# Kernel tuning notes

Hardware: AMD Instinct MI355X
Metric: run time of the kernel (lower is better)

The kernel has to match this reference:

```python
import jax, jax.numpy as jnp
import numpy as np

B, H, NC, CS, D = 4, 16, 64, 64, 64
BASE_LR = 1.0
EPS = 1e-6


def setup_inputs() -> dict:
    key = jax.random.key(0)
    ks = jax.random.split(key, 4)
    xk = jax.random.normal(ks[0], (B, H, NC, CS, D), jnp.float32)
    xv = jax.random.normal(ks[1], (B, H, NC, CS, D), jnp.float32)
    # weights/theta use the module's N(0, 0.02) init scale
    weight = 0.02 * jax.random.normal(ks[2], (H, D, D), jnp.float32)
    bias = jnp.zeros((H, 1, D), jnp.float32)
    gamma = jnp.ones((H, 1, D), jnp.float32)
    beta = jnp.zeros((H, 1, D), jnp.float32)
    theta = 0.02 * jax.random.normal(ks[3], (H, D, 1), jnp.float32)
    theta_bias = jnp.zeros((H, 1, 1), jnp.float32)
    alpha = jnp.zeros((CS,), jnp.float32)
    return dict(xk=xk, xv=xv, weight=weight, bias=bias, gamma=gamma,
                beta=beta, theta=theta, theta_bias=theta_bias, alpha=alpha)


def _ttt(xk, xv, weight, bias, gamma, beta, theta, theta_bias, alpha):
    Bq, Hq, NCq, CSq, Dq = xk.shape
    # TTTDynamicLearningGate: token_idx = clamp(1/arange + alpha, 0)
    token_idx = jnp.maximum(1.0 / jnp.arange(1, CSq + 1, dtype=xk.dtype) + alpha, 0.0)
    token_eta = token_idx[None, None, :, None]  # [1,1,CS,1]
    g = gamma[None]       # [1,H,1,D]
    bt = beta[None]       # [1,H,1,D]
    tb = theta_bias[None]  # [1,H,1,1]
    # detach(): tile slow weights over batch -> fast weights
    W0 = jnp.broadcast_to(weight[None], (Bq, Hq, Dq, Dq))
    b0 = jnp.broadcast_to(bias[None], (Bq, Hq, 1, Dq))

    def step(carry, chunk):
        W, b = carry
        xk_c, xv_c = chunk  # [B,H,CS,D]
        # lr gate: eta = token_eta * (base_lr * sigmoid(x @ theta + b) / head_dim)
        lr = jax.nn.sigmoid(jnp.einsum('bhkc,hcd->bhkd', xk_c, theta) + tb)
        eta = token_eta * (BASE_LR * lr / Dq)  # [B,H,CS,1]
        # forward through fast weights (depth = 1)
        z = xk_c @ W + b
        # multi-head LayerNorm, detailed
        mu = z.mean(-1, keepdims=True)
        var = ((z - mu) ** 2).mean(-1, keepdims=True)
        std = jnp.sqrt(var + EPS)
        x_hat = (z - mu) / std
        y = g * x_hat + bt
        # L2 reconstruction grad through LN (manual backward)
        grad_out = y - (xv_c - xk_c)
        gxh = grad_out * g
        grad_x = (Dq * gxh - gxh.sum(-1, keepdims=True)
                  - x_hat * (gxh * x_hat).sum(-1, keepdims=True)) / (Dq * std)
        # fast-weight delta + step()
        dW = jnp.einsum('bhkd,bhke->bhde', eta * xk_c, grad_x)
        db = (eta * grad_x).sum(-2, keepdims=True)
        Wn, bn = W - dW, b - db
        return (Wn, bn), xk_c @ Wn + bn

    chunks = (jnp.moveaxis(xk, 2, 0), jnp.moveaxis(xv, 2, 0))  # [NC,B,H,CS,D]
    (_, _), outs = jax.lax.scan(step, (W0, b0), chunks)
    return jnp.moveaxis(outs, 0, 2)  # [B,H,NC,CS,D]


def reference(xk, xv, weight, bias, gamma, beta, theta, theta_bias, alpha):
    return _ttt(xk, xv, weight, bias, gamma, beta, theta, theta_bias, alpha)
```

## Files before the change

### kernel.cpp

```cpp
#include <hip/hip_runtime.h>
#include <hip/hip_bf16.h>
#include <math.h>

#define NCC 64
#define CSC 64
#define DC 64
#define S 72
#define EPSF 1e-6f
#define LDS_BYTES 66816

typedef __attribute__((ext_vector_type(8))) short bf16x8;
typedef __attribute__((ext_vector_type(4))) float f32x4;
typedef __attribute__((ext_vector_type(4))) short short4v;
typedef __attribute__((ext_vector_type(2))) short short2v;

static __device__ __forceinline__ short cvt_bf16(float x) {
    union { __hip_bfloat16 b; short s; } u;
    u.b = __float2bfloat16(x);
    return u.s;
}
static __device__ __forceinline__ float bf16_to_f(unsigned hw) {
    union { unsigned u; float f; } v; v.u = hw << 16;
    return v.f;
}

#define DPP_ROR_ADD(v, N)                                                     \
    do {                                                                      \
        union { float f; int i; } _u, _r;                                     \
        _u.f = (v);                                                           \
        _r.i = __builtin_amdgcn_mov_dpp(_u.i, 0x120 + (N), 0xF, 0xF, true);   \
        (v) += _r.f;                                                          \
    } while (0)

static __device__ __forceinline__ float red16(float v) {
    DPP_ROR_ADD(v, 1);
    DPP_ROR_ADD(v, 2);
    DPP_ROR_ADD(v, 4);
    DPP_ROR_ADD(v, 8);
    return v;
}

__global__ __launch_bounds__(512, 1) void ttt_kernel(
    const float* __restrict__ xk, const float* __restrict__ xv,
    const float* __restrict__ weight, const float* __restrict__ bias,
    const float* __restrict__ gamma, const float* __restrict__ beta,
    const float* __restrict__ theta, const float* __restrict__ theta_bias,
    const float* __restrict__ alpha, float* __restrict__ out)
{
    extern __shared__ char sb[];
    auto xs_rm = (short (*)[CSC][S])(sb);
    auto xsT   = (short (*)[DC][S]) (sb + 18432);
    auto gsT   = (short (*)[S])     (sb + 36864);
    auto Gr    = (short (*)[S])     (sb + 46080);
    auto Wtb   = (short (*)[S])     (sb + 55296);
    auto dbp   = (float (*)[DC])    (sb + 64512);
    auto bs    = (float*)           (sb + 66560);

    const int t   = threadIdx.x;
    const int w   = t >> 6;
    const bool lo = (w < 4);
    const int ws  = w & 3;
    const int l   = t & 63;
    const int g   = l >> 4, la = l & 15;
    const int r0  = 16*ws + 4*g;
    const int io  = lo ? 0 : 2;
    const int ts  = 64*ws + l;
    const int bh  = blockIdx.x;
    const int h   = bh & 15;

    const size_t bh_off = (size_t)bh * NCC*CSC*DC;
    const float* xkb = xk + bh_off;
    const float* xvb = xv + bh_off;
    float*       ob  = out + bh_off;

    float gam[4], bet[4], thv[4];
#pragma unroll
    for (int n = 0; n < 4; ++n) {
        gam[n] = gamma[h*DC + 16*n + la];
        bet[n] = beta [h*DC + 16*n + la];
        thv[n] = theta[h*DC + 16*n + la];
    }
    const float tb = theta_bias[h];
    float tokk[2];
#pragma unroll
    for (int ii = 0; ii < 2; ++ii) {
        int r = r0 + io + ii;
        tokk[ii] = fmaxf(1.0f/(float)(r+1) + alpha[r], 0.0f);
    }
    if (t < DC) bs[t] = bias[h*DC + 16*(t & 3) + (t >> 2)];

    float Wreg[4][4];
    float4 xl[4];
    float xkh[4][4];
    float xvg[2][4];

#pragma unroll
    for (int ii = 0; ii < 2; ++ii)
#pragma unroll
        for (int n = 0; n < 4; ++n)
            xvg[ii][n] = xvb[(r0+io+ii)*DC + 16*n + la];

    if (lo) {
        const float* wg = weight + h*DC*DC;
#pragma unroll
        for (int i = 0; i < 4; ++i)
#pragma unroll
            for (int n = 0; n < 4; ++n)
                Wreg[i][n] = wg[(r0+i)*DC + 16*n + la];
#pragma unroll
        for (int n = 0; n < 4; ++n) {
            short4v sv;
#pragma unroll
            for (int i = 0; i < 4; ++i) sv[i] = cvt_bf16(Wreg[i][n]);
            *(short4v*)&Wtb[16*n + la][r0] = sv;
        }
#pragma unroll
        for (int i4 = 0; i4 < 4; ++i4) xl[i4] = ((const float4*)xkb)[ts + 256*i4];
#pragma unroll
        for (int i = 0; i < 4; ++i)
#pragma unroll
            for (int n = 0; n < 4; ++n)
                xkh[i][n] = xkb[(r0+i)*DC + 16*n + la];
#pragma unroll
        for (int i4 = 0; i4 < 4; ++i4) {
            int f = ts + 256*i4, k = f >> 4, j = f & 15;
            short4v s4;
            s4[0]=cvt_bf16(xl[i4].x); s4[1]=cvt_bf16(xl[i4].y);
            s4[2]=cvt_bf16(xl[i4].z); s4[3]=cvt_bf16(xl[i4].w);
            *(short4v*)&xs_rm[0][k][4*j] = s4;
        }
#pragma unroll
        for (int n = 0; n < 4; ++n) {
            short4v sv;
#pragma unroll
            for (int i = 0; i < 4; ++i) sv[i] = cvt_bf16(xkh[i][n]);
            *(short4v*)&xsT[0][16*n + la][r0] = sv;
        }
    }
    __syncthreads();

    for (int c = 0; c < NCC; ++c) {
        const int cb = c & 1, nb = cb ^ 1;
        const bool pf = (c + 1 < NCC);

        f32x4 bold = *(const f32x4*)&bs[4*la];

        const bf16x8 a0 = *(const bf16x8*)&xs_rm[cb][16*ws + la][8*g];
        const bf16x8 a1 = *(const bf16x8*)&xs_rm[cb][16*ws + la][32 + 8*g];
        f32x4 zt[4];
#pragma unroll
        for (int n = 0; n < 4; ++n) {
            bf16x8 w0 = *(const bf16x8*)&Wtb[16*n + la][8*g];
            bf16x8 w1 = *(const bf16x8*)&Wtb[16*n + la][32 + 8*g];
            f32x4 zz = {0.f,0.f,0.f,0.f};
            zz = __builtin_amdgcn_mfma_f32_16x16x32_bf16(a0, w0, zz, 0,0,0);
            zz = __builtin_amdgcn_mfma_f32_16x16x32_bf16(a1, w1, zz, 0,0,0);
            zt[n] = zz;
        }
        if (!lo) {
#pragma unroll
            for (int n = 0; n < 4; ++n) {
                bf16x8 b0 = *(const bf16x8*)&xs_rm[cb][16*n + la][8*g];
                bf16x8 b1 = *(const bf16x8*)&xs_rm[cb][16*n + la][32 + 8*g];
                f32x4 cc = {0.f,0.f,0.f,0.f};
                cc = __builtin_amdgcn_mfma_f32_16x16x32_bf16(a0, b0, cc, 0,0,0);
                cc = __builtin_amdgcn_mfma_f32_16x16x32_bf16(a1, b1, cc, 0,0,0);
                short4v sg;
#pragma unroll
                for (int i = 0; i < 4; ++i) sg[i] = cvt_bf16(-(cc[i] + 1.0f));
                *(short4v*)&Gr[16*n + la][r0] = sg;
            }
        }

        float xkq[2][4];
#pragma unroll
        for (int n = 0; n < 4; ++n) {
            unsigned pk = *(const unsigned*)&xsT[cb][16*n + la][r0 + io];
            xkq[0][n] = bf16_to_f(pk & 0xFFFFu);
            xkq[1][n] = bf16_to_f(pk >> 16);
        }

        float xvN[2][4];
        if (pf) {
            const float* xvn = xvb + (c+1)*CSC*DC;
#pragma unroll
            for (int ii = 0; ii < 2; ++ii)
#pragma unroll
                for (int n = 0; n < 4; ++n)
                    xvN[ii][n] = xvn[(r0+io+ii)*DC + 16*n + la];
            if (lo) {
                const float* xkn = xkb + (c+1)*CSC*DC;
#pragma unroll
                for (int i4 = 0; i4 < 4; ++i4) xl[i4] = ((const float4*)xkn)[ts + 256*i4];
#pragma unroll
                for (int i = 0; i < 4; ++i)
#pragma unroll
                    for (int n = 0; n < 4; ++n)
                        xkh[i][n] = xkn[(r0+i)*DC + 16*n + la];
            }
        }

        float zrow[2][4];
        if (lo) {
#pragma unroll
            for (int n = 0; n < 4; ++n) { zrow[0][n] = zt[n][0]; zrow[1][n] = zt[n][1]; }
        } else {
#pragma unroll
            for (int n = 0; n < 4; ++n) { zrow[0][n] = zt[n][2]; zrow[1][n] = zt[n][3]; }
        }

        float gsv[2][4];
#pragma unroll
        for (int ii = 0; ii < 2; ++ii) {
            float z4[4];
#pragma unroll
            for (int n = 0; n < 4; ++n) z4[n] = zrow[ii][n] + bold[n];
            float szz = red16(z4[0]*z4[0] + z4[1]*z4[1] + z4[2]*z4[2] + z4[3]*z4[3]);
            float sz  = red16(z4[0] + z4[1] + z4[2] + z4[3]);
            float thd = red16(xkq[ii][0]*thv[0] + xkq[ii][1]*thv[1] +
                              xkq[ii][2]*thv[2] + xkq[ii][3]*thv[3]);
            float mu   = sz * (1.0f/DC);
            float var  = szz*(1.0f/DC) - mu*mu;
            float rstd = rsqrtf(var + EPSF);
            float ex   = __expf(-(thd + tb));
            float lr   = __builtin_amdgcn_rcpf(1.0f + ex);
            float eta  = tokk[ii]*lr*(1.0f/DC);
            float xh[4], gxh[4], a1v = 0.f, a2v = 0.f;
#pragma unroll
            for (int n = 0; n < 4; ++n) {
                xh[n] = (z4[n]-mu)*rstd;
                float y  = fmaf(gam[n], xh[n], bet[n]);
                float go = y - xvg[ii][n] + xkq[ii][n];
                gxh[n] = go*gam[n];
                a1v += gxh[n];
                a2v = fmaf(gxh[n], xh[n], a2v);
            }
            float s1 = red16(a1v), s2 = red16(a2v);
            float sc = rstd*(1.0f/DC)*eta;
#pragma unroll
            for (int n = 0; n < 4; ++n)
                gsv[ii][n] = (64.f*gxh[n] - s1 - xh[n]*s2)*sc;
        }
#pragma unroll
        for (int n = 0; n < 4; ++n) {
            short2v sg;
            sg[0] = cvt_bf16(gsv[0][n]);
            sg[1] = cvt_bf16(gsv[1][n]);
            *(short2v*)&gsT[16*n + la][r0 + io] = sg;
        }
        float dbl[4];
#pragma unroll
        for (int n = 0; n < 4; ++n) {
            float dd = gsv[0][n] + gsv[1][n];
            dd += __shfl_xor(dd, 16);
            dd += __shfl_xor(dd, 32);
            dbl[n] = dd;
        }
        if (l < 16) {
            f32x4 dv = {dbl[0], dbl[1], dbl[2], dbl[3]};
            *(f32x4*)&dbp[w][4*la] = dv;
        }
        __syncthreads();

        if (lo) {
            const bf16x8 ax0 = *(const bf16x8*)&xsT[cb][16*ws + la][8*g];
            const bf16x8 ax1 = *(const bf16x8*)&xsT[cb][16*ws + la][32 + 8*g];
#pragma unroll
            for (int n = 0; n < 4; ++n) {
                bf16x8 q0 = *(const bf16x8*)&gsT[16*n + la][8*g];
                bf16x8 q1 = *(const bf16x8*)&gsT[16*n + la][32 + 8*g];
                f32x4 dw = {0.f,0.f,0.f,0.f};
                dw = __builtin_amdgcn_mfma_f32_16x16x32_bf16(ax0, q0, dw, 0,0,0);
                dw = __builtin_amdgcn_mfma_f32_16x16x32_bf16(ax1, q1, dw, 0,0,0);
                short4v sw;
#pragma unroll
                for (int i = 0; i < 4; ++i) {
                    Wreg[i][n] -= dw[i];
                    sw[i] = cvt_bf16(Wreg[i][n]);
                }
                *(short4v*)&Wtb[16*n + la][r0] = sw;
            }
            if (pf) {
#pragma unroll
                for (int i4 = 0; i4 < 4; ++i4) {
                    int f = ts + 256*i4, k = f >> 4, j = f & 15;
                    short4v s4;
                    s4[0]=cvt_bf16(xl[i4].x); s4[1]=cvt_bf16(xl[i4].y);
                    s4[2]=cvt_bf16(xl[i4].z); s4[3]=cvt_bf16(xl[i4].w);
                    *(short4v*)&xs_rm[nb][k][4*j] = s4;
                }
#pragma unroll
                for (int n = 0; n < 4; ++n) {
                    short4v sv;
#pragma unroll
                    for (int i = 0; i < 4; ++i) sv[i] = cvt_bf16(xkh[i][n]);
                    *(short4v*)&xsT[nb][16*n + la][r0] = sv;
                }
            }
            if (w == 0) {
                float s = dbp[0][l];
#pragma unroll
                for (int p = 1; p < 8; ++p) s += dbp[p][l];
                bs[l] -= s;
            }
        } else {
            const bf16x8 ar0 = *(const bf16x8*)&Gr[16*ws + la][8*g];
            const bf16x8 ar1 = *(const bf16x8*)&Gr[16*ws + la][32 + 8*g];
            float* oc = ob + c*CSC*DC;
#pragma unroll
            for (int n = 0; n < 4; ++n) {
                bf16x8 q0 = *(const bf16x8*)&gsT[16*n + la][8*g];
                bf16x8 q1 = *(const bf16x8*)&gsT[16*n + la][32 + 8*g];
                f32x4 og = zt[n];
                og = __builtin_amdgcn_mfma_f32_16x16x32_bf16(ar0, q0, og, 0,0,0);
                og = __builtin_amdgcn_mfma_f32_16x16x32_bf16(ar1, q1, og, 0,0,0);
#pragma unroll
                for (int i = 0; i < 4; ++i)
                    oc[(r0+i)*DC + 16*n + la] = og[i] + bold[n];
            }
        }
        if (pf) {
#pragma unroll
            for (int ii = 0; ii < 2; ++ii)
#pragma unroll
                for (int n = 0; n < 4; ++n)
                    xvg[ii][n] = xvN[ii][n];
        }
        __syncthreads();
    }
}

extern "C" void kernel_launch(void* const* d_in, const int* in_sizes, int n_in,
                              void* d_out, int out_size, void* d_ws, size_t ws_size,
                              hipStream_t stream) {
    const float* xk         = (const float*)d_in[0];
    const float* xv         = (const float*)d_in[1];
    const float* weight     = (const float*)d_in[2];
    const float* bias       = (const float*)d_in[3];
    const float* gamma      = (const float*)d_in[4];
    const float* beta       = (const float*)d_in[5];
    const float* theta      = (const float*)d_in[6];
    const float* theta_bias = (const float*)d_in[7];
    const float* alpha      = (const float*)d_in[8];
    float* out = (float*)d_out;

    (void)hipFuncSetAttribute((const void*)ttt_kernel,
                              hipFuncAttributeMaxDynamicSharedMemorySize,
                              LDS_BYTES);
    ttt_kernel<<<64, 512, LDS_BYTES, stream>>>(xk, xv, weight, bias, gamma, beta,
                                               theta, theta_bias, alpha, out);
}
```

Baseline: 141.2 us.

## Batch LayerNorm-backward reductions algebraically and move bias-grad reduction to output warps

Rewrites the LayerNorm backward so all row reductions (sum, sum of squares, theta dot, and gamma-weighted moments) are computed in one batch from z, then derives s1 and s2 in closed form. This removes the serial dependency of the second reduction round on mu/rstd, shortening the critical path of the per-chunk gradient step. It also drops the cross-lane shuffle reduction for the bias gradient, storing per-group partials to a larger LDS buffer, and has warp 4 (output side) do the final sum instead of warp 0. The trade-offs are more reductions overall, slightly different floating-point rounding, and more LDS use.

```diff
diff --git a/kernel.cpp b/kernel.cpp
--- a/kernel.cpp
+++ b/kernel.cpp
@@ -7,7 +7,7 @@
 #define DC 64
 #define S 72
 #define EPSF 1e-6f
-#define LDS_BYTES 66816
+#define LDS_BYTES 72960
 
 typedef __attribute__((ext_vector_type(8))) short bf16x8;
 typedef __attribute__((ext_vector_type(4))) float f32x4;
@@ -53,8 +53,8 @@
     auto gsT   = (short (*)[S])     (sb + 36864);
     auto Gr    = (short (*)[S])     (sb + 46080);
     auto Wtb   = (short (*)[S])     (sb + 55296);
-    auto dbp   = (float (*)[DC])    (sb + 64512);
-    auto bs    = (float*)           (sb + 66560);
+    auto dbp   = (float (*)[4][DC]) (sb + 64512);
+    auto bs    = (float*)           (sb + 72704);
 
     const int t   = threadIdx.x;
     const int w   = t >> 6;
@@ -87,6 +87,11 @@
         int r = r0 + io + ii;
         tokk[ii] = fmaxf(1.0f/(float)(r+1) + alpha[r], 0.0f);
     }
+    float a3p = 0.f;
+#pragma unroll
+    for (int n = 0; n < 4; ++n) a3p = fmaf(gam[n], gam[n], a3p);
+    const float A3 = red16(a3p);
+
     if (t < DC) bs[t] = bias[h*DC + 16*(t & 3) + (t >> 2)];
 
     float Wreg[4][4];
@@ -212,34 +217,46 @@
         float gsv[2][4];
 #pragma unroll
         for (int ii = 0; ii < 2; ++ii) {
-            float z4[4];
-#pragma unroll
-            for (int n = 0; n < 4; ++n) z4[n] = zrow[ii][n] + bold[n];
-            float szz = red16(z4[0]*z4[0] + z4[1]*z4[1] + z4[2]*z4[2] + z4[3]*z4[3]);
-            float sz  = red16(z4[0] + z4[1] + z4[2] + z4[3]);
-            float thd = red16(xkq[ii][0]*thv[0] + xkq[ii][1]*thv[1] +
-                              xkq[ii][2]*thv[2] + xkq[ii][3]*thv[3]);
+            float z4[4], cc4[4];
+#pragma unroll
+            for (int n = 0; n < 4; ++n) {
+                z4[n]  = zrow[ii][n] + bold[n];
+                cc4[n] = gam[n] * (bet[n] - xvg[ii][n] + xkq[ii][n]);
+            }
+            float p_sz=0.f, p_szz=0.f, p_thd=0.f, p_a1=0.f, p_a2=0.f, p_a4=0.f, p_a5=0.f;
+#pragma unroll
+            for (int n = 0; n < 4; ++n) {
+                float g2 = gam[n]*gam[n];
+                p_sz  += z4[n];
+                p_szz  = fmaf(z4[n], z4[n], p_szz);
+                p_thd  = fmaf(xkq[ii][n], thv[n], p_thd);
+                p_a1   = fmaf(g2, z4[n], p_a1);
+                p_a2   = fmaf(g2*z4[n], z4[n], p_a2);
+                p_a4  += cc4[n];
+                p_a5   = fmaf(cc4[n], z4[n], p_a5);
+            }
+            float sz  = red16(p_sz);
+            float szz = red16(p_szz);
+            float thd = red16(p_thd);
+            float A1  = red16(p_a1);
+            float A2  = red16(p_a2);
+            float A4  = red16(p_a4);
+            float A5  = red16(p_a5);
             float mu   = sz * (1.0f/DC);
             float var  = szz*(1.0f/DC) - mu*mu;
-            float rstd = rsqrtf(var + EPSF);
+            float r    = rsqrtf(var + EPSF);
             float ex   = __expf(-(thd + tb));
             float lr   = __builtin_amdgcn_rcpf(1.0f + ex);
             float eta  = tokk[ii]*lr*(1.0f/DC);
-            float xh[4], gxh[4], a1v = 0.f, a2v = 0.f;
-#pragma unroll
-            for (int n = 0; n < 4; ++n) {
-                xh[n] = (z4[n]-mu)*rstd;
-                float y  = fmaf(gam[n], xh[n], bet[n]);
-                float go = y - xvg[ii][n] + xkq[ii][n];
-                gxh[n] = go*gam[n];
-                a1v += gxh[n];
-                a2v = fmaf(gxh[n], xh[n], a2v);
-            }
-            float s1 = red16(a1v), s2 = red16(a2v);
-            float sc = rstd*(1.0f/DC)*eta;
-#pragma unroll
-            for (int n = 0; n < 4; ++n)
-                gsv[ii][n] = (64.f*gxh[n] - s1 - xh[n]*s2)*sc;
+            float s1 = fmaf(r, A1 - mu*A3, A4);
+            float s2 = r*r*(A2 - 2.0f*mu*A1 + mu*mu*A3) + r*(A5 - mu*A4);
+            float sc = r*(1.0f/DC)*eta;
+#pragma unroll
+            for (int n = 0; n < 4; ++n) {
+                float xh  = (z4[n]-mu)*r;
+                float gxh = fmaf(gam[n]*gam[n], xh, cc4[n]);
+                gsv[ii][n] = (64.f*gxh - s1 - xh*s2)*sc;
+            }
         }
 #pragma unroll
         for (int n = 0; n < 4; ++n) {
@@ -248,17 +265,11 @@
             sg[1] = cvt_bf16(gsv[1][n]);
             *(short2v*)&gsT[16*n + la][r0 + io] = sg;
         }
-        float dbl[4];
-#pragma unroll
-        for (int n = 0; n < 4; ++n) {
-            float dd = gsv[0][n] + gsv[1][n];
-            dd += __shfl_xor(dd, 16);
-            dd += __shfl_xor(dd, 32);
-            dbl[n] = dd;
-        }
-        if (l < 16) {
-            f32x4 dv = {dbl[0], dbl[1], dbl[2], dbl[3]};
-            *(f32x4*)&dbp[w][4*la] = dv;
+        {
+            f32x4 dv;
+#pragma unroll
+            for (int n = 0; n < 4; ++n) dv[n] = gsv[0][n] + gsv[1][n];
+            *(f32x4*)&dbp[w][g][4*la] = dv;
         }
         __syncthreads();
 
@@ -297,12 +308,6 @@
                     *(short4v*)&xsT[nb][16*n + la][r0] = sv;
                 }
             }
-            if (w == 0) {
-                float s = dbp[0][l];
-#pragma unroll
-                for (int p = 1; p < 8; ++p) s += dbp[p][l];
-                bs[l] -= s;
-            }
         } else {
             const bf16x8 ar0 = *(const bf16x8*)&Gr[16*ws + la][8*g];
             const bf16x8 ar1 = *(const bf16x8*)&Gr[16*ws + la][32 + 8*g];
@@ -317,6 +322,15 @@
 #pragma unroll
                 for (int i = 0; i < 4; ++i)
                     oc[(r0+i)*DC + 16*n + la] = og[i] + bold[n];
+            }
+            if (w == 4) {
+                float s = 0.f;
+#pragma unroll
+                for (int p = 0; p < 8; ++p)
+#pragma unroll
+                    for (int gg = 0; gg < 4; ++gg)
+                        s += dbp[p][gg][l];
+                bs[l] -= s;
             }
         }
         if (pf) {
```

Result: slower. 159.0 us (+12.7%).
